# Performance work log

Hardware: AMD Instinct MI355X
Metric: run time of the kernel (lower is better)

The kernel has to match this reference:

```python
import jax, jax.numpy as jnp
import numpy as np

B, C_IN, C_OUT, N, K = 32, 128, 128, 128, 3


def setup_inputs() -> dict:
    key = jax.random.key(0)
    k1, k2 = jax.random.split(key)
    # input image batch [B, C_in, N, N]
    x = jax.random.normal(k1, (B, C_IN, N, N), dtype=jnp.float32)
    # learned kernel, matches torch.rand init: [C_out, C_in, K, K]
    kernel = jax.random.uniform(k2, (C_OUT, C_IN, K, K), dtype=jnp.float32)
    return {"x": x, "kernel": kernel}


def reference(x, kernel):
    # BlockConv's banded block-sparse BCSR matmul is mathematically a
    # SAME-zero-padded 2D cross-correlation (no kernel flip):
    #   out[b,o,i,p] = sum_{c,k,d} kernel[o,c,k,d] * x[b,c,i+k-K//2,p+d-K//2]
    # (border blocks in _apply_constraint truncate the kernel exactly like
    #  zero padding). bias=False, so no bias term.
    return jax.lax.conv_general_dilated(
        x, kernel,
        window_strides=(1, 1),
        padding="SAME",
        dimension_numbers=("NCHW", "OIHW", "NCHW"),
    )
```

## Files before the change

kernel.cpp:

```cpp
#include <hip/hip_runtime.h>
#include <hip/hip_bf16.h>

#define B_    32
#define CIN   128
#define COUT  128
#define NN    128
#define PPAD  130
#define ROWE  (PPAD * CIN)
#define CHROW7 (PPAD * 16)
#define CH7    (4 * CHROW7)

typedef __attribute__((ext_vector_type(8))) short short8;
typedef __attribute__((ext_vector_type(4))) float float4v;

static __device__ inline unsigned short f2bf(float f) {
    union { float f; unsigned u; } v; v.f = f;
    unsigned u = v.u;
    unsigned r = u + 0x7FFFu + ((u >> 16) & 1u);
    return (unsigned short)(r >> 16);
}

static __device__ inline void gll16(const unsigned short* g, unsigned short* l) {
    __builtin_amdgcn_global_load_lds((const __attribute__((address_space(1))) unsigned int*)g,
                                     (__attribute__((address_space(3))) unsigned int*)l,
                                     16, 0, 0);
}

__global__ __launch_bounds__(256) void xpose_kernel(const float* __restrict__ x,
                                                    unsigned short* __restrict__ xT) {
    int b = blockIdx.x >> 7;
    int i = blockIdx.x & 127;
    __shared__ unsigned short tile[CIN * PPAD];
    int tid = threadIdx.x;
    const float* src = x + ((size_t)(b * CIN) * NN + i) * NN;
    #pragma unroll
    for (int e = 0; e < 64; ++e) {
        int idx = e * 256 + tid;
        int c = idx >> 7;
        int p = idx & 127;
        tile[c * PPAD + p] = f2bf(src[(size_t)c * (NN * NN) + p]);
    }
    __syncthreads();
    unsigned short* dst = xT + (size_t)(b * NN + i) * ROWE;
    #pragma unroll
    for (int e = 0; e < 32; ++e) {
        int pi = e * 256 + tid;
        int c2 = (pi & 63) * 2;
        int p  = pi >> 6;
        ushort2 v;
        v.x = tile[c2 * PPAD + p];
        v.y = tile[(c2 + 1) * PPAD + p];
        int pp = p + 1;
        int sl = (c2 >> 3) ^ (pp & 15);
        *(ushort2*)(dst + (size_t)pp * CIN + sl * 8 + (c2 & 7)) = v;
    }
    if (tid < 128) {
        dst[tid] = 0;
        dst[(size_t)129 * CIN + tid] = 0;
    }
}

__global__ __launch_bounds__(256) void ktrans_kernel(const float* __restrict__ kern,
                                                     unsigned short* __restrict__ kT2) {
    int idx = blockIdx.x * 256 + threadIdx.x;
    if (idx >= COUT * CIN * 9) return;
    int c  = idx & 127;
    int o  = (idx >> 7) & 127;
    int kd = idx >> 14;
    int k = kd / 3, d = kd % 3;
    float v = kern[(((size_t)o * CIN + c) * 3 + k) * 3 + d];
    kT2[((size_t)(kd * 16 + (c >> 3)) * 128 + o) * 8 + (c & 7)] = f2bf(v);
}

__global__ __launch_bounds__(512, 2) void conv_mfma7_kernel(const unsigned short* __restrict__ xT,
                                                            const unsigned short* __restrict__ kT2,
                                                            float* __restrict__ out) {
    __shared__ unsigned short xs[4 * ROWE];

    int wg = blockIdx.x;
    int lb = (wg & 7) * 256 + (wg >> 3);
    int b  = lb >> 6;
    int rp = lb & 63;

    int tid  = threadIdx.x;
    int lane = tid & 63;
    int wave = tid >> 6;
    int wo = wave >> 2;
    int wr = (wave >> 1) & 1;
    int wq = wave & 1;
    int ob  = wo * 64;
    int pb  = wq * 64;
    int l15 = lane & 15;
    int lg  = lane >> 4;

    {
        const unsigned short* xrow_base = xT + (size_t)b * NN * ROWE;
        #pragma unroll
        for (int s = 0; s < 17; ++s) {
            int W = s * 512 + tid;
            if (W < CH7) {
                int r    = W / CHROW7;
                int rem  = W - r * CHROW7;
                int grow = rp * 2 - 1 + r;
                int growc = grow < 0 ? 0 : (grow > NN - 1 ? NN - 1 : grow);
                gll16(xrow_base + (size_t)growc * ROWE + (size_t)rem * 8,
                      xs + (size_t)W * 8);
            }
        }
    }
    __syncthreads();

    if (rp == 0) {
        for (int W = tid; W < CHROW7; W += 512)
            *(short8*)(xs + (size_t)W * 8) = (short8)(0);
    }
    if (rp == 63) {
        for (int W = 3 * CHROW7 + tid; W < 4 * CHROW7; W += 512)
            *(short8*)(xs + (size_t)W * 8) = (short8)(0);
    }
    if (rp == 0 || rp == 63) __syncthreads();

    float4v acc[4][4];
    #pragma unroll
    for (int m = 0; m < 4; ++m)
        #pragma unroll
        for (int n = 0; n < 4; ++n)
            acc[m][n] = (float4v)(0.0f);

    #pragma unroll
    for (int kd = 0; kd < 9; ++kd) {
        const int k = kd / 3, d = kd % 3;
        const unsigned short* srow = xs + (size_t)(wr + k) * ROWE;
        #pragma unroll
        for (int cc = 0; cc < 4; ++cc) {
            const int cslot = cc * 4 + lg;
            short8 a[4], bt[4];
            #pragma unroll
            for (int m = 0; m < 4; ++m)
                a[m] = *(const short8*)(kT2 +
                    ((size_t)((kd * 16 + cslot) * 128) + ob + m * 16 + l15) * 8);
            #pragma unroll
            for (int n = 0; n < 4; ++n) {
                int pp = pb + n * 16 + l15 + d;
                bt[n] = *(const short8*)(srow + ((size_t)pp * 16 + (cslot ^ (pp & 15))) * 8);
            }
            #pragma unroll
            for (int m = 0; m < 4; ++m)
                #pragma unroll
                for (int n = 0; n < 4; ++n)
                    acc[m][n] = __builtin_amdgcn_mfma_f32_16x16x32_bf16(a[m], bt[n], acc[m][n], 0, 0, 0);
        }
    }

    int row = rp * 2 + wr;
    float* op = out + (size_t)b * COUT * NN * NN + (size_t)row * NN;
    #pragma unroll
    for (int m = 0; m < 4; ++m) {
        #pragma unroll
        for (int n = 0; n < 4; ++n) {
            int p = pb + n * 16 + l15;
            #pragma unroll
            for (int r = 0; r < 4; ++r) {
                int o = ob + m * 16 + lg * 4 + r;
                op[(size_t)o * (NN * NN) + p] = acc[m][n][r];
            }
        }
    }
}

__global__ __launch_bounds__(256) void conv_naive_kernel(const float* __restrict__ x,
                                                         const float* __restrict__ kern,
                                                         float* __restrict__ out) {
    size_t idx = (size_t)blockIdx.x * 256 + threadIdx.x;
    int p = idx & 127;
    size_t t = idx >> 7;
    int i = t & 127; t >>= 7;
    int o = t & 127;
    int b = (int)(t >> 7);
    float s = 0.f;
    for (int c = 0; c < CIN; ++c) {
        #pragma unroll
        for (int k = 0; k < 3; ++k) {
            int r = i + k - 1;
            if (r < 0 || r >= NN) continue;
            #pragma unroll
            for (int d = 0; d < 3; ++d) {
                int q = p + d - 1;
                if (q < 0 || q >= NN) continue;
                s += kern[(((size_t)o * CIN + c) * 3 + k) * 3 + d]
                   * x[(((size_t)b * CIN + c) * NN + r) * NN + q];
            }
        }
    }
    out[idx] = s;
}

extern "C" void kernel_launch(void* const* d_in, const int* in_sizes, int n_in,
                              void* d_out, int out_size, void* d_ws, size_t ws_size,
                              hipStream_t stream) {
    const float* x    = (const float*)d_in[0];
    const float* kern = (const float*)d_in[1];
    float* out = (float*)d_out;

    const size_t xT_bytes  = (size_t)B_ * NN * ROWE * 2;
    const size_t kT_bytes  = (size_t)9 * 16 * 128 * 8 * 2;

    if (ws_size >= xT_bytes + kT_bytes) {
        unsigned short* xT  = (unsigned short*)d_ws;
        unsigned short* kT2 = (unsigned short*)((char*)d_ws + xT_bytes);
        hipLaunchKernelGGL(xpose_kernel, dim3(B_ * NN), dim3(256), 0, stream, x, xT);
        hipLaunchKernelGGL(ktrans_kernel, dim3(576), dim3(256), 0, stream, kern, kT2);
        hipLaunchKernelGGL(conv_mfma7_kernel, dim3(2048), dim3(512), 0, stream, xT, kT2, out);
    } else {
        hipLaunchKernelGGL(conv_naive_kernel, dim3(67108864 / 256), dim3(256), 0, stream,
                           x, kern, out);
    }
}
```

Measured before the change: 290.6 us.

## Stream weights through triple-buffered LDS and drop padded columns from tile load

```diff
diff --git a/kernel.cpp b/kernel.cpp
--- a/kernel.cpp
+++ b/kernel.cpp
@@ -7,8 +7,8 @@
 #define NN    128
 #define PPAD  130
 #define ROWE  (PPAD * CIN)
-#define CHROW7 (PPAD * 16)
-#define CH7    (4 * CHROW7)
+#define XCH   8192
+#define ACH   512
 
 typedef __attribute__((ext_vector_type(8))) short short8;
 typedef __attribute__((ext_vector_type(4))) float float4v;
@@ -72,10 +72,10 @@
     kT2[((size_t)(kd * 16 + (c >> 3)) * 128 + o) * 8 + (c & 7)] = f2bf(v);
 }
 
-__global__ __launch_bounds__(512, 2) void conv_mfma7_kernel(const unsigned short* __restrict__ xT,
+__global__ __launch_bounds__(512, 1) void conv_mfma8_kernel(const unsigned short* __restrict__ xT,
                                                             const unsigned short* __restrict__ kT2,
                                                             float* __restrict__ out) {
-    __shared__ unsigned short xs[4 * ROWE];
+    __shared__ unsigned short xs[(XCH + 3 * ACH) * 8];
 
     int wg = blockIdx.x;
     int lb = (wg & 7) * 256 + (wg >> 3);
@@ -96,29 +96,33 @@
     {
         const unsigned short* xrow_base = xT + (size_t)b * NN * ROWE;
         #pragma unroll
-        for (int s = 0; s < 17; ++s) {
-            int W = s * 512 + tid;
-            if (W < CH7) {
-                int r    = W / CHROW7;
-                int rem  = W - r * CHROW7;
-                int grow = rp * 2 - 1 + r;
-                int growc = grow < 0 ? 0 : (grow > NN - 1 ? NN - 1 : grow);
-                gll16(xrow_base + (size_t)growc * ROWE + (size_t)rem * 8,
-                      xs + (size_t)W * 8);
-            }
-        }
-    }
-    __syncthreads();
+        for (int s = 0; s < 16; ++s) {
+            int W   = s * 512 + tid;
+            int r   = W >> 11;
+            int rem = W & 2047;
+            int grow = rp * 2 - 1 + r;
+            int growc = grow < 0 ? 0 : (grow > NN - 1 ? NN - 1 : grow);
+            gll16(xrow_base + (size_t)growc * ROWE + (size_t)(rem + 16) * 8,
+                  xs + (size_t)W * 8);
+        }
+        gll16(kT2 + (size_t)tid * 8,         xs + (size_t)(XCH + tid) * 8);
+        gll16(kT2 + (size_t)(ACH + tid) * 8, xs + (size_t)(XCH + ACH + tid) * 8);
+    }
+    asm volatile("s_waitcnt vmcnt(1)" ::: "memory");
+    __builtin_amdgcn_s_barrier();
 
     if (rp == 0) {
-        for (int W = tid; W < CHROW7; W += 512)
+        for (int W = tid; W < 2048; W += 512)
             *(short8*)(xs + (size_t)W * 8) = (short8)(0);
     }
     if (rp == 63) {
-        for (int W = 3 * CHROW7 + tid; W < 4 * CHROW7; W += 512)
+        for (int W = 3 * 2048 + tid; W < 4 * 2048; W += 512)
             *(short8*)(xs + (size_t)W * 8) = (short8)(0);
     }
-    if (rp == 0 || rp == 63) __syncthreads();
+    if (rp == 0 || rp == 63) {
+        asm volatile("s_waitcnt lgkmcnt(0)" ::: "memory");
+        __builtin_amdgcn_s_barrier();
+    }
 
     float4v acc[4][4];
     #pragma unroll
@@ -130,25 +134,37 @@
     #pragma unroll
     for (int kd = 0; kd < 9; ++kd) {
         const int k = kd / 3, d = kd % 3;
-        const unsigned short* srow = xs + (size_t)(wr + k) * ROWE;
         #pragma unroll
         for (int cc = 0; cc < 4; ++cc) {
-            const int cslot = cc * 4 + lg;
+            const int ph = kd * 4 + cc;
             short8 a[4], bt[4];
+            const unsigned short* ab = xs + (size_t)(XCH + (ph % 3) * ACH) * 8;
             #pragma unroll
             for (int m = 0; m < 4; ++m)
-                a[m] = *(const short8*)(kT2 +
-                    ((size_t)((kd * 16 + cslot) * 128) + ob + m * 16 + l15) * 8);
+                a[m] = *(const short8*)(ab + ((size_t)lg * 128 + ob + m * 16 + l15) * 8);
+            const unsigned short* srow = xs + (size_t)(wr + k) * 2048 * 8;
             #pragma unroll
             for (int n = 0; n < 4; ++n) {
-                int pp = pb + n * 16 + l15 + d;
-                bt[n] = *(const short8*)(srow + ((size_t)pp * 16 + (cslot ^ (pp & 15))) * 8);
-            }
+                int q  = pb + n * 16 + l15 + d - 1;
+                int qc = q < 0 ? 0 : (q > 127 ? 127 : q);
+                int j  = (cc * 4 + lg) ^ ((qc + 1) & 15);
+                short8 v = *(const short8*)(srow + ((size_t)qc * 16 + j) * 8);
+                bt[n] = (q < 0 || q > 127) ? (short8)(0) : v;
+            }
+            {
+                const int pn = (ph + 2 > 35) ? 35 : (ph + 2);
+                gll16(kT2 + ((size_t)pn * ACH + tid) * 8,
+                      xs + (size_t)(XCH + (pn % 3) * ACH + tid) * 8);
+            }
+            __builtin_amdgcn_s_setprio(1);
             #pragma unroll
             for (int m = 0; m < 4; ++m)
                 #pragma unroll
                 for (int n = 0; n < 4; ++n)
                     acc[m][n] = __builtin_amdgcn_mfma_f32_16x16x32_bf16(a[m], bt[n], acc[m][n], 0, 0, 0);
+            __builtin_amdgcn_s_setprio(0);
+            asm volatile("s_waitcnt vmcnt(1)" ::: "memory");
+            __builtin_amdgcn_s_barrier();
         }
     }
 
@@ -210,7 +226,7 @@
         unsigned short* kT2 = (unsigned short*)((char*)d_ws + xT_bytes);
         hipLaunchKernelGGL(xpose_kernel, dim3(B_ * NN), dim3(256), 0, stream, x, xT);
         hipLaunchKernelGGL(ktrans_kernel, dim3(576), dim3(256), 0, stream, kern, kT2);
-        hipLaunchKernelGGL(conv_mfma7_kernel, dim3(2048), dim3(512), 0, stream, xT, kT2, out);
+        hipLaunchKernelGGL(conv_mfma8_kernel, dim3(2048), dim3(512), 0, stream, xT, kT2, out);
     } else {
         hipLaunchKernelGGL(conv_naive_kernel, dim3(67108864 / 256), dim3(256), 0, stream,
                            x, kern, out);
```

Measured after the change: 258.9 us. -10.9%, faster.

## Fuse input transpose and bf16 conversion into conv kernel with staged weight pipeline

Applied to the files above, without the earlier changes.

```diff
diff --git a/kernel.cpp b/kernel.cpp
--- a/kernel.cpp
+++ b/kernel.cpp
@@ -6,12 +6,13 @@
 #define COUT  128
 #define NN    128
 #define PPAD  130
-#define ROWE  (PPAD * CIN)
-#define CHROW7 (PPAD * 16)
-#define CH7    (4 * CHROW7)
+#define CHROW 2080
+#define XCHT  (4 * CHROW)
+#define ACH   512
 
 typedef __attribute__((ext_vector_type(8))) short short8;
 typedef __attribute__((ext_vector_type(4))) float float4v;
+typedef __attribute__((ext_vector_type(4))) float f32x4;
 
 static __device__ inline unsigned short f2bf(float f) {
     union { float f; unsigned u; } v; v.f = f;
@@ -24,40 +25,6 @@
     __builtin_amdgcn_global_load_lds((const __attribute__((address_space(1))) unsigned int*)g,
                                      (__attribute__((address_space(3))) unsigned int*)l,
                                      16, 0, 0);
-}
-
-__global__ __launch_bounds__(256) void xpose_kernel(const float* __restrict__ x,
-                                                    unsigned short* __restrict__ xT) {
-    int b = blockIdx.x >> 7;
-    int i = blockIdx.x & 127;
-    __shared__ unsigned short tile[CIN * PPAD];
-    int tid = threadIdx.x;
-    const float* src = x + ((size_t)(b * CIN) * NN + i) * NN;
-    #pragma unroll
-    for (int e = 0; e < 64; ++e) {
-        int idx = e * 256 + tid;
-        int c = idx >> 7;
-        int p = idx & 127;
-        tile[c * PPAD + p] = f2bf(src[(size_t)c * (NN * NN) + p]);
-    }
-    __syncthreads();
-    unsigned short* dst = xT + (size_t)(b * NN + i) * ROWE;
-    #pragma unroll
-    for (int e = 0; e < 32; ++e) {
-        int pi = e * 256 + tid;
-        int c2 = (pi & 63) * 2;
-        int p  = pi >> 6;
-        ushort2 v;
-        v.x = tile[c2 * PPAD + p];
-        v.y = tile[(c2 + 1) * PPAD + p];
-        int pp = p + 1;
-        int sl = (c2 >> 3) ^ (pp & 15);
-        *(ushort2*)(dst + (size_t)pp * CIN + sl * 8 + (c2 & 7)) = v;
-    }
-    if (tid < 128) {
-        dst[tid] = 0;
-        dst[(size_t)129 * CIN + tid] = 0;
-    }
 }
 
 __global__ __launch_bounds__(256) void ktrans_kernel(const float* __restrict__ kern,
@@ -72,10 +39,11 @@
     kT2[((size_t)(kd * 16 + (c >> 3)) * 128 + o) * 8 + (c & 7)] = f2bf(v);
 }
 
-__global__ __launch_bounds__(512, 2) void conv_mfma7_kernel(const unsigned short* __restrict__ xT,
-                                                            const unsigned short* __restrict__ kT2,
-                                                            float* __restrict__ out) {
-    __shared__ unsigned short xs[4 * ROWE];
+__global__ __launch_bounds__(512, 1) void conv_fused_kernel(
+        const float* __restrict__ x,
+        const unsigned short* __restrict__ kT2,
+        float* __restrict__ out) {
+    __shared__ unsigned short xs[(XCHT + 3 * ACH) * 8];
 
     int wg = blockIdx.x;
     int lb = (wg & 7) * 256 + (wg >> 3);
@@ -93,32 +61,65 @@
     int l15 = lane & 15;
     int lg  = lane >> 4;
 
-    {
-        const unsigned short* xrow_base = xT + (size_t)b * NN * ROWE;
-        #pragma unroll
-        for (int s = 0; s < 17; ++s) {
-            int W = s * 512 + tid;
-            if (W < CH7) {
-                int r    = W / CHROW7;
-                int rem  = W - r * CHROW7;
-                int grow = rp * 2 - 1 + r;
-                int growc = grow < 0 ? 0 : (grow > NN - 1 ? NN - 1 : grow);
-                gll16(xrow_base + (size_t)growc * ROWE + (size_t)rem * 8,
-                      xs + (size_t)W * 8);
-            }
-        }
-    }
-    __syncthreads();
-
-    if (rp == 0) {
-        for (int W = tid; W < CHROW7; W += 512)
+    const int c0 = (tid >> 4) * 4;
+    const int q  = tid & 15;
+    const float* xb = x + (size_t)b * CIN * NN * NN;
+    const int g0c = (rp == 0)  ? 0   : rp * 2 - 1;
+    const int g1  = rp * 2;
+    const int g2  = rp * 2 + 1;
+    const int g3c = (rp == 63) ? 127 : rp * 2 + 2;
+
+    #define TWRITE(r, p, v0, v1, v2, v3)                                        \
+        {                                                                       \
+            int pp_ = (p) + 1;                                                  \
+            size_t ch_ = (size_t)(r) * CHROW + (size_t)pp_ * 16                 \
+                       + ((c0 >> 3) ^ (pp_ & 15));                              \
+            union { unsigned short u[4]; uint2 w; } pk_;                        \
+            pk_.u[0] = f2bf(v0); pk_.u[1] = f2bf(v1);                           \
+            pk_.u[2] = f2bf(v2); pk_.u[3] = f2bf(v3);                           \
+            *(uint2*)(xs + ch_ * 8 + (c0 & 7)) = pk_.w;                         \
+        }
+
+    f32x4 L0[8], L1[8];
+    #pragma unroll
+    for (int j = 0; j < 4; ++j)
+        #pragma unroll
+        for (int h = 0; h < 2; ++h)
+            L0[j * 2 + h] = *(const f32x4*)(xb + ((size_t)(c0 + j) * NN + g0c) * NN + q * 8 + h * 4);
+    #pragma unroll
+    for (int j = 0; j < 4; ++j)
+        #pragma unroll
+        for (int h = 0; h < 2; ++h)
+            L1[j * 2 + h] = *(const f32x4*)(xb + ((size_t)(c0 + j) * NN + g1) * NN + q * 8 + h * 4);
+    gll16(kT2 + (size_t)tid * 8,         xs + (size_t)(XCHT + tid) * 8);
+    gll16(kT2 + (size_t)(ACH + tid) * 8, xs + (size_t)(XCHT + ACH + tid) * 8);
+    asm volatile("s_waitcnt vmcnt(1)" ::: "memory");
+
+    if (rp != 0) {
+        #pragma unroll
+        for (int h = 0; h < 2; ++h)
+            #pragma unroll
+            for (int i = 0; i < 4; ++i)
+                TWRITE(0, q * 8 + h * 4 + i, L0[0 * 2 + h][i], L0[1 * 2 + h][i],
+                                             L0[2 * 2 + h][i], L0[3 * 2 + h][i]);
+    } else {
+        for (int W = tid; W < CHROW; W += 512)
             *(short8*)(xs + (size_t)W * 8) = (short8)(0);
     }
-    if (rp == 63) {
-        for (int W = 3 * CHROW7 + tid; W < 4 * CHROW7; W += 512)
-            *(short8*)(xs + (size_t)W * 8) = (short8)(0);
-    }
-    if (rp == 0 || rp == 63) __syncthreads();
+    #pragma unroll
+    for (int h = 0; h < 2; ++h)
+        #pragma unroll
+        for (int i = 0; i < 4; ++i)
+            TWRITE(1, q * 8 + h * 4 + i, L1[0 * 2 + h][i], L1[1 * 2 + h][i],
+                                         L1[2 * 2 + h][i], L1[3 * 2 + h][i]);
+    if (tid < 128) {
+        int r_  = tid >> 5;
+        int pp_ = ((tid >> 4) & 1) ? 129 : 0;
+        int j_  = tid & 15;
+        *(short8*)(xs + ((size_t)r_ * CHROW + (size_t)pp_ * 16 + j_) * 8) = (short8)(0);
+    }
+    asm volatile("s_waitcnt lgkmcnt(0)" ::: "memory");
+    __builtin_amdgcn_s_barrier();
 
     float4v acc[4][4];
     #pragma unroll
@@ -127,30 +128,80 @@
         for (int n = 0; n < 4; ++n)
             acc[m][n] = (float4v)(0.0f);
 
-    #pragma unroll
-    for (int kd = 0; kd < 9; ++kd) {
+    f32x4 L2[8], L3[8];
+
+    #pragma unroll
+    for (int ph = 0; ph < 36; ++ph) {
+        const int kd = ph >> 2, cc = ph & 3;
         const int k = kd / 3, d = kd % 3;
-        const unsigned short* srow = xs + (size_t)(wr + k) * ROWE;
-        #pragma unroll
-        for (int cc = 0; cc < 4; ++cc) {
-            const int cslot = cc * 4 + lg;
-            short8 a[4], bt[4];
+        if (ph + 2 <= 35)
+            gll16(kT2 + ((size_t)(ph + 2) * ACH + tid) * 8,
+                  xs + (size_t)(XCHT + ((ph + 2) % 3) * ACH + tid) * 8);
+        if (ph == 0 || ph == 1) {
+            #pragma unroll
+            for (int j = 0; j < 4; ++j)
+                L2[j * 2 + ph] = *(const f32x4*)(xb + ((size_t)(c0 + j) * NN + g2) * NN + q * 8 + ph * 4);
+        }
+        if (ph == 2 || ph == 3) {
+            const int h = ph - 2;
+            #pragma unroll
+            for (int j = 0; j < 4; ++j)
+                L3[j * 2 + h] = *(const f32x4*)(xb + ((size_t)(c0 + j) * NN + g3c) * NN + q * 8 + h * 4);
+        }
+        if (ph == 4) {
+            #pragma unroll
+            for (int h = 0; h < 2; ++h)
+                #pragma unroll
+                for (int i = 0; i < 4; ++i)
+                    TWRITE(2, q * 8 + h * 4 + i, L2[0 * 2 + h][i], L2[1 * 2 + h][i],
+                                                 L2[2 * 2 + h][i], L2[3 * 2 + h][i]);
+        }
+        if (ph == 6) {
+            if (rp != 63) {
+                #pragma unroll
+                for (int h = 0; h < 2; ++h)
+                    #pragma unroll
+                    for (int i = 0; i < 4; ++i)
+                        TWRITE(3, q * 8 + h * 4 + i, L3[0 * 2 + h][i], L3[1 * 2 + h][i],
+                                                     L3[2 * 2 + h][i], L3[3 * 2 + h][i]);
+            } else {
+                for (int W = 3 * CHROW + tid; W < 4 * CHROW; W += 512)
+                    *(short8*)(xs + (size_t)W * 8) = (short8)(0);
+            }
+        }
+        short8 a[4], bt[4];
+        {
+            const unsigned short* ab = xs + (size_t)(XCHT + (ph % 3) * ACH) * 8;
             #pragma unroll
             for (int m = 0; m < 4; ++m)
-                a[m] = *(const short8*)(kT2 +
-                    ((size_t)((kd * 16 + cslot) * 128) + ob + m * 16 + l15) * 8);
+                a[m] = *(const short8*)(ab + ((size_t)lg * 128 + ob + m * 16 + l15) * 8);
+            const unsigned short* srow = xs + (size_t)(wr + k) * CHROW * 8;
             #pragma unroll
             for (int n = 0; n < 4; ++n) {
                 int pp = pb + n * 16 + l15 + d;
-                bt[n] = *(const short8*)(srow + ((size_t)pp * 16 + (cslot ^ (pp & 15))) * 8);
-            }
-            #pragma unroll
-            for (int m = 0; m < 4; ++m)
-                #pragma unroll
-                for (int n = 0; n < 4; ++n)
-                    acc[m][n] = __builtin_amdgcn_mfma_f32_16x16x32_bf16(a[m], bt[n], acc[m][n], 0, 0, 0);
-        }
-    }
+                bt[n] = *(const short8*)(srow + ((size_t)pp * 16 + ((cc * 4 + lg) ^ (pp & 15))) * 8);
+            }
+        }
+        __builtin_amdgcn_s_setprio(1);
+        #pragma unroll
+        for (int m = 0; m < 4; ++m)
+            #pragma unroll
+            for (int n = 0; n < 4; ++n)
+                acc[m][n] = __builtin_amdgcn_mfma_f32_16x16x32_bf16(a[m], bt[n], acc[m][n], 0, 0, 0);
+        __builtin_amdgcn_s_setprio(0);
+        if (ph == 4 || ph == 6)
+            asm volatile("s_waitcnt lgkmcnt(0)" ::: "memory");
+        if      (ph == 0) asm volatile("s_waitcnt vmcnt(5)" ::: "memory");
+        else if (ph == 1) asm volatile("s_waitcnt vmcnt(9)" ::: "memory");
+        else if (ph == 2) asm volatile("s_waitcnt vmcnt(8)" ::: "memory");
+        else if (ph == 3) asm volatile("s_waitcnt vmcnt(8)" ::: "memory");
+        else if (ph == 4) asm volatile("s_waitcnt vmcnt(5)" ::: "memory");
+        else if (ph == 5) asm volatile("s_waitcnt vmcnt(1)" ::: "memory");
+        else if (ph == 34) asm volatile("s_waitcnt vmcnt(0)" ::: "memory");
+        else if (ph <= 33) asm volatile("s_waitcnt vmcnt(1)" ::: "memory");
+        if (ph < 35) __builtin_amdgcn_s_barrier();
+    }
+    #undef TWRITE
 
     int row = rp * 2 + wr;
     float* op = out + (size_t)b * COUT * NN * NN + (size_t)row * NN;
@@ -185,10 +236,10 @@
             if (r < 0 || r >= NN) continue;
             #pragma unroll
             for (int d = 0; d < 3; ++d) {
-                int q = p + d - 1;
-                if (q < 0 || q >= NN) continue;
+                int q2 = p + d - 1;
+                if (q2 < 0 || q2 >= NN) continue;
                 s += kern[(((size_t)o * CIN + c) * 3 + k) * 3 + d]
-                   * x[(((size_t)b * CIN + c) * NN + r) * NN + q];
+                   * x[(((size_t)b * CIN + c) * NN + r) * NN + q2];
             }
         }
     }
@@ -202,15 +253,12 @@
     const float* kern = (const float*)d_in[1];
     float* out = (float*)d_out;
 
-    const size_t xT_bytes  = (size_t)B_ * NN * ROWE * 2;
-    const size_t kT_bytes  = (size_t)9 * 16 * 128 * 8 * 2;
-
-    if (ws_size >= xT_bytes + kT_bytes) {
-        unsigned short* xT  = (unsigned short*)d_ws;
-        unsigned short* kT2 = (unsigned short*)((char*)d_ws + xT_bytes);
-        hipLaunchKernelGGL(xpose_kernel, dim3(B_ * NN), dim3(256), 0, stream, x, xT);
+    const size_t kT_bytes = (size_t)9 * 16 * 128 * 8 * 2;
+
+    if (ws_size >= kT_bytes) {
+        unsigned short* kT2 = (unsigned short*)d_ws;
         hipLaunchKernelGGL(ktrans_kernel, dim3(576), dim3(256), 0, stream, kern, kT2);
-        hipLaunchKernelGGL(conv_mfma7_kernel, dim3(2048), dim3(512), 0, stream, xT, kT2, out);
+        hipLaunchKernelGGL(conv_fused_kernel, dim3(2048), dim3(512), 0, stream, x, kT2, out);
     } else {
         hipLaunchKernelGGL(conv_naive_kernel, dim3(67108864 / 256), dim3(256), 0, stream,
                            x, kern, out);
```

New measurement: 271.5 us. -6.6%, faster.
